# Kernel optimization log

Hardware: AMD Instinct MI355X
Metric: run time of the kernel (lower is better)

The kernel has to match this reference:

```python
import jax, jax.numpy as jnp
import numpy as np

CHANNELS = 512
NUM_HEADS = 4
GROUPS = 32
EPS = 1e-5


def setup_inputs() -> dict:
    key = jax.random.key(0)
    ks = jax.random.split(key, 7)
    C = CHANNELS
    x = jax.random.normal(ks[0], (16, C, 32, 32), dtype=jnp.float32)
    norm_w = jnp.ones((C,), dtype=jnp.float32)
    norm_b = jnp.zeros((C,), dtype=jnp.float32)
    qkv_w = jax.random.normal(ks[1], (3 * C, C), dtype=jnp.float32) * (C ** -0.5)
    qkv_b = jnp.zeros((3 * C,), dtype=jnp.float32)
    proj_w = jax.random.normal(ks[2], (C, C), dtype=jnp.float32) * (C ** -0.5)
    proj_b = jnp.zeros((C,), dtype=jnp.float32)
    return {"x": x, "norm_w": norm_w, "norm_b": norm_b,
            "qkv_w": qkv_w, "qkv_b": qkv_b,
            "proj_w": proj_w, "proj_b": proj_b}


def reference(x, norm_w, norm_b, qkv_w, qkv_b, proj_w, proj_b):
    B, C, H, W = x.shape
    heads = NUM_HEADS
    hd = C // heads  # head dim
    N = H * W

    # GroupNorm(32, C): normalize over (C/32, H, W) per group, then per-channel affine
    xg = x.reshape(B, GROUPS, -1)
    mu = jnp.mean(xg, axis=-1, keepdims=True)
    var = jnp.var(xg, axis=-1, keepdims=True)
    h = ((xg - mu) * jax.lax.rsqrt(var + EPS)).reshape(B, C, H, W)
    h = h * norm_w[None, :, None, None] + norm_b[None, :, None, None]

    # 1x1 conv qkv: [B,C,H,W] -> [B,3C,H,W]
    qkv = jnp.einsum('oc,bchw->bohw', qkv_w, h) + qkv_b[None, :, None, None]
    qkv = qkv.reshape(B, 3, heads, hd, N)
    q, k, v = qkv[:, 0], qkv[:, 1], qkv[:, 2]  # each [B, heads, hd, N]

    scale = hd ** -0.5
    attn = jnp.einsum('bhcn,bhcm->bhnm', q, k) * scale  # [B, heads, N, N]
    attn = jax.nn.softmax(attn, axis=-1)
    h = jnp.einsum('bhnm,bhcm->bhcn', attn, v).reshape(B, C, H, W)

    # 1x1 conv proj + residual
    h = jnp.einsum('oc,bchw->bohw', proj_w, h) + proj_b[None, :, None, None]
    return x + h
```

## Files before the change

kernel.cpp:

```cpp
#include <hip/hip_runtime.h>

typedef __bf16 v8bf __attribute__((ext_vector_type(8)));
typedef float  v4f  __attribute__((ext_vector_type(4)));
typedef unsigned short u16;

__device__ __forceinline__ u16 f2bf(float f){
  __bf16 h = (__bf16)f;
  union { __bf16 h; u16 u; } c; c.h = h; return c.u;
}
__device__ __forceinline__ v4f v4zero(){ v4f z; z[0]=0.f; z[1]=0.f; z[2]=0.f; z[3]=0.f; return z; }

#define MFMA16(a,b,c) __builtin_amdgcn_mfma_f32_16x16x32_bf16((a),(b),(c),0,0,0)

__device__ __forceinline__ void gl_lds16(const u16* g, u16* l){
  __builtin_amdgcn_global_load_lds((const __attribute__((address_space(1))) void*)g,
                                   (__attribute__((address_space(3))) void*)l, 16, 0, 0);
}

__global__ __launch_bounds__(256) void cvt_kernel(const float* __restrict__ src, u16* __restrict__ dst, int n){
  int i = (blockIdx.x*256 + threadIdx.x)*4;
  if (i < n){
    float4 v = *(const float4*)(src + i);
    ushort4 o;
    o.x = f2bf(v.x); o.y = f2bf(v.y); o.z = f2bf(v.z); o.w = f2bf(v.w);
    *(ushort4*)(dst + i) = o;
  }
}

__global__ __launch_bounds__(256) void gn_stats_kernel(const float* __restrict__ x, float* __restrict__ stats){
  const float* base = x + (size_t)blockIdx.x * 16384;
  float s = 0.f, ss = 0.f;
  #pragma unroll
  for (int it = 0; it < 16; ++it){
    float4 v = *(const float4*)(base + it*1024 + threadIdx.x*4);
    s  += v.x + v.y + v.z + v.w;
    ss += v.x*v.x + v.y*v.y + v.z*v.z + v.w*v.w;
  }
  #pragma unroll
  for (int off = 32; off > 0; off >>= 1){ s += __shfl_down(s, off); ss += __shfl_down(ss, off); }
  __shared__ float red[8];
  int w = threadIdx.x >> 6;
  if ((threadIdx.x & 63) == 0){ red[w] = s; red[4+w] = ss; }
  __syncthreads();
  if (threadIdx.x == 0){
    float S  = red[0]+red[1]+red[2]+red[3];
    float SS = red[4]+red[5]+red[6]+red[7];
    float mean = S * (1.f/16384.f);
    float var  = SS * (1.f/16384.f) - mean*mean;
    stats[blockIdx.x*2]   = mean;
    stats[blockIdx.x*2+1] = rsqrtf(var + 1e-5f);
  }
}

__global__ __launch_bounds__(256) void gn_apply_kernel(const float* __restrict__ x, const float* __restrict__ nw,
                                                       const float* __restrict__ nb, const float* __restrict__ stats,
                                                       u16* __restrict__ h_t){
  __shared__ u16 tile[32*520];
  int b = blockIdx.y, n0 = blockIdx.x*32, tid = threadIdx.x;
  int cr = tid >> 2, nn = (tid & 3)*8;
  #pragma unroll
  for (int p = 0; p < 8; ++p){
    int c = p*64 + cr;
    const float* px = x + (size_t)(b*512 + c)*1024 + n0 + nn;
    float4 u0 = *(const float4*)(px);
    float4 u1 = *(const float4*)(px + 4);
    int g = c >> 4;
    float mean = stats[(b*32+g)*2], rstd = stats[(b*32+g)*2+1];
    float wv = nw[c], bv = nb[c];
    float vals[8] = {u0.x,u0.y,u0.z,u0.w,u1.x,u1.y,u1.z,u1.w};
    #pragma unroll
    for (int e = 0; e < 8; ++e)
      tile[(nn+e)*520 + c] = f2bf((vals[e] - mean)*rstd*wv + bv);
  }
  __syncthreads();
  #pragma unroll
  for (int p = 0; p < 8; ++p){
    int n  = p*4 + (tid >> 6);
    int c0 = (tid & 63)*8;
    *(int4*)(h_t + ((size_t)b*1024 + n0 + n)*512 + c0) = *(int4*)(tile + n*520 + c0);
  }
}

__global__ __launch_bounds__(256,2) void gemm_qkv_kernel(
    const u16* __restrict__ A,
    const u16* __restrict__ B,
    const float* __restrict__ bias,
    u16* __restrict__ qk_t, u16* __restrict__ v_ws)
{
  __shared__ u16 smem[24576];
  const int tid = threadIdx.x, w = tid>>6, lane = tid&63, col = lane&15, quad = lane>>4;
  const int m0 = blockIdx.y*128;
  const int n0 = blockIdx.x*256;
  const int b  = blockIdx.z;
  const int lr = lane>>2;
  const int gsw = ((lane&3) ^ (lr&3))*8;
  const u16* Ag = A + ((size_t)b*1024 + m0 + w*32 + lr)*512 + gsw;
  const u16* Bg = B + (size_t)(n0 + w*64 + lr)*512 + gsw;
  const int mw = (w&1)*64, nw = (w>>1)*128;
  const int fsw = (quad ^ (col&3))*8;

  v4f acc[4][8];
  #pragma unroll
  for (int i=0;i<4;++i)
    #pragma unroll
    for (int j=0;j<8;++j) acc[i][j] = v4zero();

  {
    u16* Ab = smem + (w*32)*32;
    u16* Bb = smem + 4096 + (w*64)*32;
    #pragma unroll
    for (int p = 0; p < 2; ++p) gl_lds16(Ag + (size_t)(p*16)*512, Ab + p*512);
    #pragma unroll
    for (int p = 0; p < 4; ++p) gl_lds16(Bg + (size_t)(p*16)*512, Bb + p*512);
  }

  for (int kt = 0; kt < 16; ++kt){
    __syncthreads();
    if (kt < 15){
      u16* Ab = smem + ((kt+1)&1)*12288 + (w*32)*32;
      u16* Bb = smem + ((kt+1)&1)*12288 + 4096 + (w*64)*32;
      int ko = (kt+1)*32;
      #pragma unroll
      for (int p = 0; p < 2; ++p) gl_lds16(Ag + (size_t)(p*16)*512 + ko, Ab + p*512);
      #pragma unroll
      for (int p = 0; p < 4; ++p) gl_lds16(Bg + (size_t)(p*16)*512 + ko, Bb + p*512);
    }
    const u16* As = smem + (kt&1)*12288;
    const u16* Bs = As + 4096;
    v8bf a[4], bb[8];
    #pragma unroll
    for (int i = 0; i < 4; ++i) a[i]  = *(const v8bf*)(As + (mw+i*16+col)*32 + fsw);
    #pragma unroll
    for (int j = 0; j < 8; ++j) bb[j] = *(const v8bf*)(Bs + (nw+j*16+col)*32 + fsw);
    #pragma unroll
    for (int i = 0; i < 4; ++i)
      #pragma unroll
      for (int j = 0; j < 8; ++j)
        acc[i][j] = MFMA16(a[i], bb[j], acc[i][j]);
  }
  __syncthreads();

  float bc[8];
  #pragma unroll
  for (int j = 0; j < 8; ++j)
    bc[j] = bias[n0 + nw + j*16 + col];

  if (n0 < 1024){
    u16* Cs = smem + w*(64*72);
    #pragma unroll
    for (int half = 0; half < 2; ++half){
      #pragma unroll
      for (int i = 0; i < 4; ++i)
        #pragma unroll
        for (int jj = 0; jj < 4; ++jj)
          #pragma unroll
          for (int r = 0; r < 4; ++r)
            Cs[(i*16+quad*4+r)*72 + jj*16+col] = f2bf(acc[i][half*4+jj][r] + bc[half*4+jj]);
      u16* dst = qk_t + (size_t)b*1024*1024;
      #pragma unroll
      for (int p = 0; p < 8; ++p){
        int rl = p*8 + (lane>>3), cl = (lane&7)*8;
        *(int4*)(dst + (size_t)(m0+mw+rl)*1024 + n0+nw+half*64+cl) = *(int4*)(Cs + rl*72 + cl);
      }
    }
  } else {
    u16* Ct = smem + w*(64*80);
    #pragma unroll
    for (int half = 0; half < 2; ++half){
      #pragma unroll
      for (int i = 0; i < 4; ++i)
        #pragma unroll
        for (int jj = 0; jj < 4; ++jj)
          #pragma unroll
          for (int r = 0; r < 4; ++r)
            Ct[(jj*16+col)*80 + i*16+quad*4+r] = f2bf(acc[i][half*4+jj][r] + bc[half*4+jj]);
      u16* dst = v_ws + (size_t)b*512*1024;
      #pragma unroll
      for (int p = 0; p < 8; ++p){
        int rl = p*8 + (lane>>3), cl = (lane&7)*8;
        *(int4*)(dst + (size_t)(n0-1024 + nw + half*64 + rl)*1024 + m0+mw+cl) = *(int4*)(Ct + rl*80 + cl);
      }
    }
  }
}

__global__ __launch_bounds__(256,2) void gemm_bt_kernel(
    const u16* __restrict__ A, long long sA,
    const u16* __restrict__ B, long long sB,
    u16* __restrict__ Cbf, float* __restrict__ Cf, long long sC,
    const float* __restrict__ bias_row,
    const float* __restrict__ bias_col,
    const float* __restrict__ residf, long long sR,
    int M, int N, int K)
{
  __shared__ u16 smem[32768];
  const int tid = threadIdx.x, w = tid>>6, lane = tid&63, col = lane&15, quad = lane>>4;
  const int m0 = blockIdx.y*128, n0 = blockIdx.x*128;
  const int lr8 = lane>>3;
  const int gsw = ((lane&7) ^ lr8)*8;
  const u16* Ag = A + (size_t)blockIdx.z*sA + (size_t)(m0 + w*32 + lr8)*K + gsw;
  const u16* Bg = B + (size_t)blockIdx.z*sB + (size_t)(n0 + w*32 + lr8)*K + gsw;
  const int mw = (w&1)*64, nw = (w>>1)*64;
  const int csw = col&7;
  const int nt = K >> 6;

  v4f acc[4][4];
  #pragma unroll
  for (int i=0;i<4;++i)
    #pragma unroll
    for (int j=0;j<4;++j) acc[i][j] = v4zero();

  {
    u16* Ab = smem + (w*32)*64;
    u16* Bb = smem + 8192 + (w*32)*64;
    #pragma unroll
    for (int p = 0; p < 4; ++p){
      gl_lds16(Ag + (size_t)(p*8)*K, Ab + p*512);
      gl_lds16(Bg + (size_t)(p*8)*K, Bb + p*512);
    }
  }

  for (int kt = 0; kt < nt; ++kt){
    __syncthreads();
    if (kt+1 < nt){
      u16* Ab = smem + ((kt+1)&1)*16384 + (w*32)*64;
      u16* Bb = smem + ((kt+1)&1)*16384 + 8192 + (w*32)*64;
      int ko = (kt+1)*64;
      #pragma unroll
      for (int p = 0; p < 4; ++p){
        gl_lds16(Ag + (size_t)(p*8)*K + ko, Ab + p*512);
        gl_lds16(Bg + (size_t)(p*8)*K + ko, Bb + p*512);
      }
    }
    const u16* As = smem + (kt&1)*16384;
    const u16* Bs = As + 8192;
    #pragma unroll
    for (int kh = 0; kh < 2; ++kh){
      const int fs = ((kh*4 + quad) ^ csw)*8;
      v8bf a[4], bb[4];
      #pragma unroll
      for (int i = 0; i < 4; ++i) a[i]  = *(const v8bf*)(As + (mw+i*16+col)*64 + fs);
      #pragma unroll
      for (int j = 0; j < 4; ++j) bb[j] = *(const v8bf*)(Bs + (nw+j*16+col)*64 + fs);
      #pragma unroll
      for (int i = 0; i < 4; ++i)
        #pragma unroll
        for (int j = 0; j < 4; ++j)
          acc[i][j] = MFMA16(a[i], bb[j], acc[i][j]);
    }
  }
  __syncthreads();

  float br[4][4], bc[4];
  #pragma unroll
  for (int i = 0; i < 4; ++i)
    #pragma unroll
    for (int r = 0; r < 4; ++r)
      br[i][r] = bias_row ? bias_row[m0+mw+i*16+quad*4+r] : 0.f;
  #pragma unroll
  for (int j = 0; j < 4; ++j)
    bc[j] = bias_col ? bias_col[n0+nw+j*16+col] : 0.f;

  if (Cf){
    float* Cb = Cf + (size_t)blockIdx.z*sC;
    const float* Rb = residf ? residf + (size_t)blockIdx.z*sR : nullptr;
    #pragma unroll
    for (int i = 0; i < 4; ++i)
      #pragma unroll
      for (int r = 0; r < 4; ++r){
        int row = m0+mw+i*16+quad*4+r;
        #pragma unroll
        for (int j = 0; j < 4; ++j){
          size_t goff = (size_t)row*N + n0+nw+j*16+col;
          float val = acc[i][j][r] + br[i][r] + bc[j];
          if (Rb) val += Rb[goff];
          Cb[goff] = val;
        }
      }
  } else {
    u16* Cs = smem + w*(64*72);
    #pragma unroll
    for (int i = 0; i < 4; ++i)
      #pragma unroll
      for (int j = 0; j < 4; ++j)
        #pragma unroll
        for (int r = 0; r < 4; ++r)
          Cs[(i*16+quad*4+r)*72 + j*16+col] = f2bf(acc[i][j][r] + br[i][r] + bc[j]);
    __syncthreads();
    u16* Cb = Cbf + (size_t)blockIdx.z*sC;
    #pragma unroll
    for (int p = 0; p < 8; ++p){
      int rl = p*8 + (lane>>3), cl = (lane&7)*8;
      size_t goff = (size_t)(m0+mw+rl)*N + n0+nw+cl;
      *(int4*)(Cb + goff) = *(int4*)(Cs + rl*72 + cl);
    }
  }
}

__global__ __launch_bounds__(256,2) void attn_kernel(const u16* __restrict__ qk, const u16* __restrict__ vv,
                                                     u16* __restrict__ outp){
  __shared__ u16 smem[32768];
  u16* Ks = smem;
  u16* Vs = smem + 8192;
  u16* Ps = smem + 8192 + 16384;
  const int id = blockIdx.x;
  const int qt = id >> 6, bh = id & 63, b = bh >> 2, h = bh & 3;
  const int n0 = qt*128;
  const int tid = threadIdx.x, w = tid>>6, lane = tid&63, col = lane&15, quad = lane>>4;
  const size_t bq = (size_t)b*1024*1024;
  const float scale2 = 0.12751742f;

  v8bf aq[2][4];
  #pragma unroll
  for (int i = 0; i < 2; ++i)
    #pragma unroll
    for (int kk = 0; kk < 4; ++kk)
      aq[i][kk] = *(const v8bf*)(qk + bq + (size_t)(n0 + w*32 + i*16 + col)*1024 + h*128 + kk*32 + quad*8);

  v4f o[2][8];
  #pragma unroll
  for (int i=0;i<2;++i)
    #pragma unroll
    for (int j=0;j<8;++j) o[i][j] = v4zero();
  float lsum[8];
  #pragma unroll
  for (int r=0;r<8;++r) lsum[r] = 0.f;

  const int krow = w*4 + (lane>>4);
  const int kgr  = (lane&15) ^ (krow&7);
  const u16* kg_base = qk + bq + (size_t)krow*1024 + 512 + h*128 + kgr*8;
  u16* kl_base = Ks + (w*4)*128;
  const int vrow = w*8 + (lane>>3);
  const int vgr  = (lane&7) ^ (vrow&7);
  const u16* vg_base = vv + ((size_t)b*512 + h*128 + vrow)*1024 + vgr*8;

  #pragma unroll
  for (int p = 0; p < 4; ++p)
    gl_lds16(kg_base + (size_t)(p*16)*1024, kl_base + p*16*128);
  #pragma unroll
  for (int p = 0; p < 4; ++p)
    gl_lds16(vg_base + (size_t)(p*32)*1024, Vs + (w*8 + p*32)*64);

  for (int t = 0; t < 16; ++t){
    const int mt = t*64;
    __syncthreads();

    v4f s[2][4];
    #pragma unroll
    for (int i=0;i<2;++i)
      #pragma unroll
      for (int j=0;j<4;++j) s[i][j] = v4zero();
    #pragma unroll
    for (int kk = 0; kk < 4; ++kk){
      v8bf bk[4];
      #pragma unroll
      for (int j = 0; j < 4; ++j){
        int r = j*16 + col;
        int g = (kk*4 + quad) ^ (r&7);
        bk[j] = *(const v8bf*)(Ks + (r<<7) + (g<<3));
      }
      #pragma unroll
      for (int i = 0; i < 2; ++i)
        #pragma unroll
        for (int j = 0; j < 4; ++j)
          s[i][j] = MFMA16(aq[i][kk], bk[j], s[i][j]);
    }
    __syncthreads();

    if (t < 15){
      int mt2 = mt + 64;
      #pragma unroll
      for (int p = 0; p < 4; ++p)
        gl_lds16(kg_base + (size_t)(mt2 + p*16)*1024, kl_base + p*16*128);
      u16* vl = Vs + (((t+1)&1)<<13) + (w*8)*64;
      #pragma unroll
      for (int p = 0; p < 4; ++p)
        gl_lds16(vg_base + (size_t)(p*32)*1024 + mt2, vl + p*32*64);
    }

    #pragma unroll
    for (int i = 0; i < 2; ++i)
      #pragma unroll
      for (int r = 0; r < 4; ++r){
        float p0 = __builtin_amdgcn_exp2f(s[i][0][r]*scale2);
        float p1 = __builtin_amdgcn_exp2f(s[i][1][r]*scale2);
        float p2 = __builtin_amdgcn_exp2f(s[i][2][r]*scale2);
        float p3 = __builtin_amdgcn_exp2f(s[i][3][r]*scale2);
        lsum[i*4+r] += (p0+p1) + (p2+p3);
        int rr = w*32 + i*16 + quad*4 + r;
        int key = (rr ^ (rr>>2)) & 7;
        Ps[(rr<<6) + (((0 ^ key))<<3) + (col&7) + ((col>>3)? ((1^key)<<3)-((0^key)<<3) : 0)] = f2bf(p0);
        Ps[(rr<<6) + ((((16*1+col)>>3) ^ key)<<3) + (col&7)] = f2bf(p1);
        Ps[(rr<<6) + ((((16*2+col)>>3) ^ key)<<3) + (col&7)] = f2bf(p2);
        Ps[(rr<<6) + ((((16*3+col)>>3) ^ key)<<3) + (col&7)] = f2bf(p3);
      }
    #pragma unroll
    for (int i = 0; i < 2; ++i)
      #pragma unroll
      for (int r = 0; r < 4; ++r){
        int rr = w*32 + i*16 + quad*4 + r;
        int key = (rr ^ (rr>>2)) & 7;
        float p0 = __builtin_amdgcn_exp2f(s[i][0][r]*scale2);
        Ps[(rr<<6) + ((((col)>>3) ^ key)<<3) + (col&7)] = f2bf(p0);
      }

    const u16* Vc = Vs + ((t&1)<<13);
    #pragma unroll
    for (int kk = 0; kk < 2; ++kk){
      v8bf ap[2];
      #pragma unroll
      for (int i = 0; i < 2; ++i){
        int rr = w*32 + i*16 + col;
        int key = (rr ^ (rr>>2)) & 7;
        int g = (kk*4 + quad) ^ key;
        ap[i] = *(const v8bf*)(Ps + (rr<<6) + (g<<3));
      }
      #pragma unroll
      for (int j = 0; j < 8; ++j){
        int vr = j*16 + col;
        int g = (kk*4 + quad) ^ (vr&7);
        v8bf bv = *(const v8bf*)(Vc + (vr<<6) + (g<<3));
        #pragma unroll
        for (int i = 0; i < 2; ++i) o[i][j] = MFMA16(ap[i], bv, o[i][j]);
      }
    }
  }
  __syncthreads();

  #pragma unroll
  for (int i = 0; i < 2; ++i)
    #pragma unroll
    for (int r = 0; r < 4; ++r){
      float l = lsum[i*4+r];
      l += __shfl_xor(l, 1);
      l += __shfl_xor(l, 2);
      l += __shfl_xor(l, 4);
      l += __shfl_xor(l, 8);
      float inv = 1.f / l;
      #pragma unroll
      for (int j = 0; j < 8; ++j) o[i][j][r] *= inv;
    }

  #pragma unroll
  for (int i = 0; i < 2; ++i)
    #pragma unroll
    for (int j = 0; j < 8; ++j)
      #pragma unroll
      for (int r = 0; r < 4; ++r){
        int rr = w*32 + i*16 + quad*4 + r;
        int c  = j*16 + col;
        smem[(rr<<7) + ((((c>>3) ^ (rr&7))<<3)) + (c&7)] = f2bf(o[i][j][r]);
      }
  __syncthreads();
  #pragma unroll
  for (int p = 0; p < 8; ++p){
    int nr = p*16 + (tid>>4);
    int gc = (tid&15) ^ (nr&7);
    *(int4*)(outp + ((size_t)b*1024 + n0 + nr)*512 + h*128 + ((tid&15)<<3)) =
      *(int4*)(smem + (nr<<7) + (gc<<3));
  }
}

extern "C" void kernel_launch(void* const* d_in, const int* in_sizes, int n_in,
                              void* d_out, int out_size, void* d_ws, size_t ws_size,
                              hipStream_t stream){
  const float* x      = (const float*)d_in[0];
  const float* norm_w = (const float*)d_in[1];
  const float* norm_b = (const float*)d_in[2];
  const float* qkv_w  = (const float*)d_in[3];
  const float* qkv_b  = (const float*)d_in[4];
  const float* proj_w = (const float*)d_in[5];
  const float* proj_b = (const float*)d_in[6];
  float* out = (float*)d_out;

  u16* h_t   = (u16*)d_ws;
  u16* qk_t  = h_t  + (size_t)16*1024*512;
  u16* v_ws  = qk_t + (size_t)16*1024*1024;
  u16* wq_bf = v_ws + (size_t)16*512*1024;
  u16* wp_bf = wq_bf + (size_t)1536*512;
  float* stats = (float*)(wp_bf + (size_t)512*512);
  u16* attnout = h_t;

  cvt_kernel<<<768, 256, 0, stream>>>(qkv_w, wq_bf, 1536*512);
  cvt_kernel<<<256, 256, 0, stream>>>(proj_w, wp_bf, 512*512);
  gn_stats_kernel<<<512, 256, 0, stream>>>(x, stats);
  gn_apply_kernel<<<dim3(32,16), 256, 0, stream>>>(x, norm_w, norm_b, stats, h_t);

  gemm_qkv_kernel<<<dim3(6,8,16), 256, 0, stream>>>(h_t, wq_bf, qkv_b, qk_t, v_ws);

  attn_kernel<<<512, 256, 0, stream>>>(qk_t, v_ws, attnout);

  gemm_bt_kernel<<<dim3(8,4,16), 256, 0, stream>>>(
      wp_bf, 0, attnout, (long long)1024*512,
      nullptr, out, (long long)512*1024, proj_b, nullptr, x, (long long)512*1024, 512, 1024, 512);
}
```

Before: 215.7 us.

## Fuse GroupNorm passes, merge weight casts, double-buffer K and dedupe softmax stores

Merges the two weight-conversion launches into one kernel, and fuses GroupNorm statistics and apply into a single kernel that keeps the group's 16x1024 slice in shared memory. This removes a second read of x from global memory and two launches. In attention, K tiles are now double-buffered like V, so the next tile's prefetch starts before the QK^T MFMAs and one barrier per iteration goes away. The redundant second write of P0 is also removed. The cost is more LDS per attention block (80KB) and a large LDS footprint in the GroupNorm kernel (about 66KB), which may reduce occupancy.

```diff
diff --git a/kernel.cpp b/kernel.cpp
--- a/kernel.cpp
+++ b/kernel.cpp
@@ -17,67 +17,66 @@
                                    (__attribute__((address_space(3))) void*)l, 16, 0, 0);
 }
 
-__global__ __launch_bounds__(256) void cvt_kernel(const float* __restrict__ src, u16* __restrict__ dst, int n){
+__global__ __launch_bounds__(256) void cvt2_kernel(const float* __restrict__ a, u16* __restrict__ da, int na,
+                                                   const float* __restrict__ b, u16* __restrict__ db, int nb){
   int i = (blockIdx.x*256 + threadIdx.x)*4;
-  if (i < n){
-    float4 v = *(const float4*)(src + i);
-    ushort4 o;
-    o.x = f2bf(v.x); o.y = f2bf(v.y); o.z = f2bf(v.z); o.w = f2bf(v.w);
-    *(ushort4*)(dst + i) = o;
-  }
-}
-
-__global__ __launch_bounds__(256) void gn_stats_kernel(const float* __restrict__ x, float* __restrict__ stats){
-  const float* base = x + (size_t)blockIdx.x * 16384;
+  const float* s; u16* d; int off;
+  if (i < na){ s = a; d = da; off = i; }
+  else { off = i - na; if (off >= nb) return; s = b; d = db; }
+  float4 v = *(const float4*)(s + off);
+  ushort4 o;
+  o.x = f2bf(v.x); o.y = f2bf(v.y); o.z = f2bf(v.z); o.w = f2bf(v.w);
+  *(ushort4*)(d + off) = o;
+}
+
+__global__ __launch_bounds__(256) void gn_fused_kernel(const float* __restrict__ x, const float* __restrict__ nw,
+                                                       const float* __restrict__ nb, u16* __restrict__ h_t){
+  __shared__ float xs[16*1028 + 16];
+  const int bg = blockIdx.x, b = bg >> 5, g = bg & 31, c0 = g*16;
+  const int tid = threadIdx.x;
+  const float* base = x + (size_t)(b*512 + c0)*1024;
+
   float s = 0.f, ss = 0.f;
   #pragma unroll
   for (int it = 0; it < 16; ++it){
-    float4 v = *(const float4*)(base + it*1024 + threadIdx.x*4);
+    float4 v = *(const float4*)(base + it*1024 + tid*4);
     s  += v.x + v.y + v.z + v.w;
     ss += v.x*v.x + v.y*v.y + v.z*v.z + v.w*v.w;
+    *(float4*)(xs + it*1028 + tid*4) = v;
   }
   #pragma unroll
   for (int off = 32; off > 0; off >>= 1){ s += __shfl_down(s, off); ss += __shfl_down(ss, off); }
-  __shared__ float red[8];
-  int w = threadIdx.x >> 6;
-  if ((threadIdx.x & 63) == 0){ red[w] = s; red[4+w] = ss; }
-  __syncthreads();
-  if (threadIdx.x == 0){
+  float* red = xs + 16*1028;
+  int w = tid >> 6;
+  if ((tid & 63) == 0){ red[w] = s; red[4+w] = ss; }
+  __syncthreads();
+  if (tid == 0){
     float S  = red[0]+red[1]+red[2]+red[3];
     float SS = red[4]+red[5]+red[6]+red[7];
     float mean = S * (1.f/16384.f);
     float var  = SS * (1.f/16384.f) - mean*mean;
-    stats[blockIdx.x*2]   = mean;
-    stats[blockIdx.x*2+1] = rsqrtf(var + 1e-5f);
-  }
-}
-
-__global__ __launch_bounds__(256) void gn_apply_kernel(const float* __restrict__ x, const float* __restrict__ nw,
-                                                       const float* __restrict__ nb, const float* __restrict__ stats,
-                                                       u16* __restrict__ h_t){
-  __shared__ u16 tile[32*520];
-  int b = blockIdx.y, n0 = blockIdx.x*32, tid = threadIdx.x;
-  int cr = tid >> 2, nn = (tid & 3)*8;
+    red[8] = mean;
+    red[9] = rsqrtf(var + 1e-5f);
+  }
+  __syncthreads();
+  const float mean = red[8], rstd = red[9];
+
+  const int half = tid & 1, nbase = tid >> 1;
+  float wv[8], bv[8];
+  #pragma unroll
+  for (int cl = 0; cl < 8; ++cl){
+    int c = c0 + half*8 + cl;
+    wv[cl] = nw[c] * rstd;
+    bv[cl] = nb[c] - mean * wv[cl];
+  }
   #pragma unroll
   for (int p = 0; p < 8; ++p){
-    int c = p*64 + cr;
-    const float* px = x + (size_t)(b*512 + c)*1024 + n0 + nn;
-    float4 u0 = *(const float4*)(px);
-    float4 u1 = *(const float4*)(px + 4);
-    int g = c >> 4;
-    float mean = stats[(b*32+g)*2], rstd = stats[(b*32+g)*2+1];
-    float wv = nw[c], bv = nb[c];
-    float vals[8] = {u0.x,u0.y,u0.z,u0.w,u1.x,u1.y,u1.z,u1.w};
-    #pragma unroll
-    for (int e = 0; e < 8; ++e)
-      tile[(nn+e)*520 + c] = f2bf((vals[e] - mean)*rstd*wv + bv);
-  }
-  __syncthreads();
-  #pragma unroll
-  for (int p = 0; p < 8; ++p){
-    int n  = p*4 + (tid >> 6);
-    int c0 = (tid & 63)*8;
-    *(int4*)(h_t + ((size_t)b*1024 + n0 + n)*512 + c0) = *(int4*)(tile + n*520 + c0);
+    int n = nbase + p*128;
+    alignas(16) u16 tmp[8];
+    #pragma unroll
+    for (int cl = 0; cl < 8; ++cl)
+      tmp[cl] = f2bf(xs[(half*8 + cl)*1028 + n] * wv[cl] + bv[cl]);
+    *(int4*)(h_t + ((size_t)b*1024 + n)*512 + c0 + half*8) = *(int4*)tmp;
   }
 }
 
@@ -299,10 +298,10 @@
 
 __global__ __launch_bounds__(256,2) void attn_kernel(const u16* __restrict__ qk, const u16* __restrict__ vv,
                                                      u16* __restrict__ outp){
-  __shared__ u16 smem[32768];
+  __shared__ u16 smem[40960];
   u16* Ks = smem;
-  u16* Vs = smem + 8192;
-  u16* Ps = smem + 8192 + 16384;
+  u16* Vs = smem + 16384;
+  u16* Ps = smem + 32768;
   const int id = blockIdx.x;
   const int qt = id >> 6, bh = id & 63, b = bh >> 2, h = bh & 3;
   const int n0 = qt*128;
@@ -329,22 +328,34 @@
   const int krow = w*4 + (lane>>4);
   const int kgr  = (lane&15) ^ (krow&7);
   const u16* kg_base = qk + bq + (size_t)krow*1024 + 512 + h*128 + kgr*8;
-  u16* kl_base = Ks + (w*4)*128;
   const int vrow = w*8 + (lane>>3);
   const int vgr  = (lane&7) ^ (vrow&7);
   const u16* vg_base = vv + ((size_t)b*512 + h*128 + vrow)*1024 + vgr*8;
 
   #pragma unroll
   for (int p = 0; p < 4; ++p)
-    gl_lds16(kg_base + (size_t)(p*16)*1024, kl_base + p*16*128);
+    gl_lds16(kg_base + (size_t)(p*16)*1024, Ks + (w*4)*128 + p*2048);
   #pragma unroll
   for (int p = 0; p < 4; ++p)
-    gl_lds16(vg_base + (size_t)(p*32)*1024, Vs + (w*8 + p*32)*64);
+    gl_lds16(vg_base + (size_t)(p*32)*1024, Vs + (w*8)*64 + p*2048);
 
   for (int t = 0; t < 16; ++t){
     const int mt = t*64;
     __syncthreads();
 
+    if (t < 15){
+      int mt2 = mt + 64;
+      u16* kl = Ks + (((t+1)&1)<<13) + (w*4)*128;
+      #pragma unroll
+      for (int p = 0; p < 4; ++p)
+        gl_lds16(kg_base + (size_t)(mt2 + p*16)*1024, kl + p*2048);
+      u16* vl = Vs + (((t+1)&1)<<13) + (w*8)*64;
+      #pragma unroll
+      for (int p = 0; p < 4; ++p)
+        gl_lds16(vg_base + (size_t)(p*32)*1024 + mt2, vl + p*2048);
+    }
+
+    const u16* Kc = Ks + ((t&1)<<13);
     v4f s[2][4];
     #pragma unroll
     for (int i=0;i<2;++i)
@@ -357,7 +368,7 @@
       for (int j = 0; j < 4; ++j){
         int r = j*16 + col;
         int g = (kk*4 + quad) ^ (r&7);
-        bk[j] = *(const v8bf*)(Ks + (r<<7) + (g<<3));
+        bk[j] = *(const v8bf*)(Kc + (r<<7) + (g<<3));
       }
       #pragma unroll
       for (int i = 0; i < 2; ++i)
@@ -365,43 +376,22 @@
         for (int j = 0; j < 4; ++j)
           s[i][j] = MFMA16(aq[i][kk], bk[j], s[i][j]);
     }
-    __syncthreads();
-
-    if (t < 15){
-      int mt2 = mt + 64;
-      #pragma unroll
-      for (int p = 0; p < 4; ++p)
-        gl_lds16(kg_base + (size_t)(mt2 + p*16)*1024, kl_base + p*16*128);
-      u16* vl = Vs + (((t+1)&1)<<13) + (w*8)*64;
-      #pragma unroll
-      for (int p = 0; p < 4; ++p)
-        gl_lds16(vg_base + (size_t)(p*32)*1024 + mt2, vl + p*32*64);
-    }
-
-    #pragma unroll
-    for (int i = 0; i < 2; ++i)
-      #pragma unroll
-      for (int r = 0; r < 4; ++r){
-        float p0 = __builtin_amdgcn_exp2f(s[i][0][r]*scale2);
-        float p1 = __builtin_amdgcn_exp2f(s[i][1][r]*scale2);
-        float p2 = __builtin_amdgcn_exp2f(s[i][2][r]*scale2);
-        float p3 = __builtin_amdgcn_exp2f(s[i][3][r]*scale2);
-        lsum[i*4+r] += (p0+p1) + (p2+p3);
-        int rr = w*32 + i*16 + quad*4 + r;
-        int key = (rr ^ (rr>>2)) & 7;
-        Ps[(rr<<6) + (((0 ^ key))<<3) + (col&7) + ((col>>3)? ((1^key)<<3)-((0^key)<<3) : 0)] = f2bf(p0);
-        Ps[(rr<<6) + ((((16*1+col)>>3) ^ key)<<3) + (col&7)] = f2bf(p1);
-        Ps[(rr<<6) + ((((16*2+col)>>3) ^ key)<<3) + (col&7)] = f2bf(p2);
-        Ps[(rr<<6) + ((((16*3+col)>>3) ^ key)<<3) + (col&7)] = f2bf(p3);
-      }
+
     #pragma unroll
     for (int i = 0; i < 2; ++i)
       #pragma unroll
       for (int r = 0; r < 4; ++r){
         int rr = w*32 + i*16 + quad*4 + r;
         int key = (rr ^ (rr>>2)) & 7;
-        float p0 = __builtin_amdgcn_exp2f(s[i][0][r]*scale2);
-        Ps[(rr<<6) + ((((col)>>3) ^ key)<<3) + (col&7)] = f2bf(p0);
+        int rbase = (rr<<6) + (col&7);
+        float ps[4];
+        #pragma unroll
+        for (int j = 0; j < 4; ++j){
+          float pv = __builtin_amdgcn_exp2f(s[i][j][r]*scale2);
+          ps[j] = pv;
+          Ps[rbase + ((((j*16+col)>>3) ^ key)<<3)] = f2bf(pv);
+        }
+        lsum[i*4+r] += (ps[0]+ps[1]) + (ps[2]+ps[3]);
       }
 
     const u16* Vc = Vs + ((t&1)<<13);
@@ -478,13 +468,10 @@
   u16* v_ws  = qk_t + (size_t)16*1024*1024;
   u16* wq_bf = v_ws + (size_t)16*512*1024;
   u16* wp_bf = wq_bf + (size_t)1536*512;
-  float* stats = (float*)(wp_bf + (size_t)512*512);
   u16* attnout = h_t;
 
-  cvt_kernel<<<768, 256, 0, stream>>>(qkv_w, wq_bf, 1536*512);
-  cvt_kernel<<<256, 256, 0, stream>>>(proj_w, wp_bf, 512*512);
-  gn_stats_kernel<<<512, 256, 0, stream>>>(x, stats);
-  gn_apply_kernel<<<dim3(32,16), 256, 0, stream>>>(x, norm_w, norm_b, stats, h_t);
+  cvt2_kernel<<<1024, 256, 0, stream>>>(qkv_w, wq_bf, 1536*512, proj_w, wp_bf, 512*512);
+  gn_fused_kernel<<<512, 256, 0, stream>>>(x, norm_w, norm_b, h_t);
 
   gemm_qkv_kernel<<<dim3(6,8,16), 256, 0, stream>>>(h_t, wq_bf, qkv_b, qk_t, v_ws);
 
```

New measurement: 208.1 us. -3.5%, faster.
